# Optimization experiments

Hardware: AMD Instinct MI355X
Metric: run time of the kernel (lower is better)

Reference implementation:

```python
import jax, jax.numpy as jnp
import numpy as np

SEQ, BATCH, IN_DIM, HID, OUT = 512, 256, 300, 256, 2


def setup_inputs() -> dict:
    key = jax.random.key(0)
    ks = jax.random.split(key, 7)
    s_ih = 1.0 / np.sqrt(HID)
    return {
        "x": jax.random.normal(ks[0], (SEQ, BATCH, IN_DIM), jnp.float32),
        "W_ih": jax.random.uniform(ks[1], (HID, IN_DIM), jnp.float32, -s_ih, s_ih),
        "W_hh": jax.random.uniform(ks[2], (HID, HID), jnp.float32, -s_ih, s_ih),
        "b_ih": jax.random.uniform(ks[3], (HID,), jnp.float32, -s_ih, s_ih),
        "b_hh": jax.random.uniform(ks[4], (HID,), jnp.float32, -s_ih, s_ih),
        "W_fc": jax.random.uniform(ks[5], (OUT, HID), jnp.float32, -s_ih, s_ih),
        "b_fc": jax.random.uniform(ks[6], (OUT,), jnp.float32, -s_ih, s_ih),
    }


def reference(x, W_ih, W_hh, b_ih, b_hh, W_fc, b_fc):
    # Precompute input projection for all timesteps at once: [T, B, H]
    xp = jnp.einsum('tbi,hi->tbh', x, W_ih) + b_ih + b_hh

    def step(h, xt):
        h_new = jnp.tanh(xt + h @ W_hh.T)
        return h_new, None

    h0 = jnp.zeros((x.shape[1], W_hh.shape[0]), x.dtype)
    hT, _ = jax.lax.scan(step, h0, xp)  # hT: [B, H]
    # Dropout(0.3) is identity in eval mode.
    logits = hT @ W_fc.T + b_fc  # [B, 2]
    return jax.nn.log_softmax(logits, axis=-1)
```

## Files before the change

kernel.cpp:

```cpp
#include <hip/hip_runtime.h>
#include <hip/hip_bf16.h>
#include <cstdint>
#include <cstddef>

#define SEQ 512
#define BATCH 256
#define IN_DIM 300
#define HID 256

typedef __attribute__((ext_vector_type(8))) short bf16x8;
typedef __attribute__((ext_vector_type(4))) float f32x4;
typedef __attribute__((ext_vector_type(4))) unsigned int u32x4;

__device__ __forceinline__ unsigned short f2bf(float f) {
  union { float f; unsigned int u; } v; v.f = f;
  unsigned int u = v.u;
  return (unsigned short)((u + 0x7fffu + ((u >> 16) & 1u)) >> 16);
}
__device__ __forceinline__ unsigned short f2bf_fast(float f) {
  union { float f; unsigned int u; } v; v.f = f;
  return (unsigned short)((v.u + 0x8000u) >> 16);
}
__device__ __forceinline__ float bitsf(unsigned int u) {
  union { unsigned int u; float f; } v; v.u = u; return v.f;
}
__device__ __forceinline__ unsigned int cvtpk(float lo, float hi) {
  union { __hip_bfloat162 h; unsigned int u; } c;
  c.h = __float22bfloat162_rn(make_float2(lo, hi));
  return c.u;
}
__device__ __forceinline__ bf16x8 cvt8(float a0,float a1,float a2,float a3,
                                       float a4,float a5,float a6,float a7) {
  union { __hip_bfloat162 h2[4]; bf16x8 v; } c;
  c.h2[0] = __float22bfloat162_rn(make_float2(a0, a1));
  c.h2[1] = __float22bfloat162_rn(make_float2(a2, a3));
  c.h2[2] = __float22bfloat162_rn(make_float2(a4, a5));
  c.h2[3] = __float22bfloat162_rn(make_float2(a6, a7));
  return c.v;
}
__device__ __forceinline__ void barrier_lgkm() {
  asm volatile("s_waitcnt lgkmcnt(0)" ::: "memory");
  __builtin_amdgcn_s_barrier();
  asm volatile("" ::: "memory");
}

struct F8 { float v[8]; };
__device__ __forceinline__ F8 load_x8(const float* __restrict__ xrow, int k0, int ac) {
  F8 r;
  if (k0 + ac + 8 <= IN_DIM) {
    float2 p0 = *(const float2*)(xrow + k0 + ac + 0);
    float2 p1 = *(const float2*)(xrow + k0 + ac + 2);
    float2 p2 = *(const float2*)(xrow + k0 + ac + 4);
    float2 p3 = *(const float2*)(xrow + k0 + ac + 6);
    r.v[0]=p0.x; r.v[1]=p0.y; r.v[2]=p1.x; r.v[3]=p1.y;
    r.v[4]=p2.x; r.v[5]=p2.y; r.v[6]=p3.x; r.v[7]=p3.y;
  } else {
    #pragma unroll
    for (int j = 0; j < 8; ++j)
      r.v[j] = (k0 + ac + j < IN_DIM) ? xrow[k0 + ac + j] : 0.f;
  }
  return r;
}

__global__ __launch_bounds__(256) void conv_wih(const float* __restrict__ w,
                                                unsigned short* __restrict__ w_bf) {
  int idx = blockIdx.x * 256 + threadIdx.x;
  int j    = idx & 7;
  int l15  = (idx >> 3) & 15;
  int quad = (idx >> 7) & 3;
  int t    = idx >> 9;
  int n16  = t / 10;
  int kc   = t - n16 * 10;
  int n = n16 * 16 + l15;
  int k = kc * 32 + quad * 8 + j;
  float v = (k < IN_DIM) ? w[n * IN_DIM + k] : 0.f;
  w_bf[idx] = f2bf(v);
}

__global__ __launch_bounds__(512, 2) void gemm_xp(const float* __restrict__ x,
    const unsigned short* __restrict__ w_bf, const float* __restrict__ b_ih,
    const float* __restrict__ b_hh, unsigned int* __restrict__ xp2)
{
  __shared__ unsigned int a_lds[2][128][20];
  const int tid  = threadIdx.x;
  const int wave = tid >> 6;
  const int lane = tid & 63;
  const int l15  = lane & 15;
  const int quad = lane >> 4;
  const long m0  = (long)blockIdx.x * 128;

  bf16x8 wf[2][10];
  #pragma unroll
  for (int nt = 0; nt < 2; ++nt) {
    const unsigned short* wp =
        w_bf + ((size_t)((wave*2 + nt)*10)*4 + quad)*16*8 + (size_t)l15*8;
    #pragma unroll
    for (int kc = 0; kc < 10; ++kc)
      wf[nt][kc] = *(const bf16x8*)(wp + (size_t)kc*4*16*8);
  }

  f32x4 acc[8][2];
  #pragma unroll
  for (int mt = 0; mt < 8; ++mt) {
    acc[mt][0] = (f32x4){0.f, 0.f, 0.f, 0.f};
    acc[mt][1] = (f32x4){0.f, 0.f, 0.f, 0.f};
  }

  const int ar = tid >> 2;
  const int ac = (tid & 3) * 8;
  const float* xrow = x + (size_t)(m0 + ar) * IN_DIM;

  F8 av[2];
  av[0] = load_x8(xrow, 0, ac);
  av[1] = load_x8(xrow, 32, ac);
  {
    u32x4 pk;
    pk.x = cvtpk(av[0].v[0], av[0].v[1]);
    pk.y = cvtpk(av[0].v[2], av[0].v[3]);
    pk.z = cvtpk(av[0].v[4], av[0].v[5]);
    pk.w = cvtpk(av[0].v[6], av[0].v[7]);
    *(u32x4*)&a_lds[0][ar][(tid & 3) * 4] = pk;
  }
  barrier_lgkm();

  #pragma unroll
  for (int kc = 0; kc < 10; ++kc) {
    const int cur = kc & 1;
    bf16x8 afr[8];
    #pragma unroll
    for (int mt = 0; mt < 8; ++mt)
      afr[mt] = *(const bf16x8*)&a_lds[cur][mt*16 + l15][quad*4];
    if (kc < 9) {
      const int s = (kc + 1) & 1;
      u32x4 pk;
      pk.x = cvtpk(av[s].v[0], av[s].v[1]);
      pk.y = cvtpk(av[s].v[2], av[s].v[3]);
      pk.z = cvtpk(av[s].v[4], av[s].v[5]);
      pk.w = cvtpk(av[s].v[6], av[s].v[7]);
      *(u32x4*)&a_lds[s][ar][(tid & 3) * 4] = pk;
    }
    if (kc < 8)
      av[kc & 1] = load_x8(xrow, (kc + 2) * 32, ac);
    #pragma unroll
    for (int mt = 0; mt < 8; ++mt) {
      acc[mt][0] = __builtin_amdgcn_mfma_f32_16x16x32_bf16(afr[mt], wf[0][kc], acc[mt][0], 0, 0, 0);
      acc[mt][1] = __builtin_amdgcn_mfma_f32_16x16x32_bf16(afr[mt], wf[1][kc], acc[mt][1], 0, 0, 0);
    }
    barrier_lgkm();
  }

  const int t  = (int)(blockIdx.x >> 1);
  const int b4 = ((int)blockIdx.x & 1) * 32;
  #pragma unroll
  for (int nt = 0; nt < 2; ++nt) {
    const int n = wave*32 + nt*16 + l15;
    const float kb = 2.0f * (b_ih[n] + b_hh[n]);
    const int tid_lo = wave*64 + nt*16 + l15;
    #pragma unroll
    for (int mt = 0; mt < 8; ++mt) {
      const int g = b4 + mt*4 + quad;
      const size_t base = ((size_t)t*64 + g) * 512;
      float y0 = fmaf(2.0f, acc[mt][nt][0], kb);
      float y1 = fmaf(2.0f, acc[mt][nt][1], kb);
      float y2 = fmaf(2.0f, acc[mt][nt][2], kb);
      float y3 = fmaf(2.0f, acc[mt][nt][3], kb);
      xp2[base + tid_lo]      = cvtpk(y0, y1);
      xp2[base + tid_lo + 32] = cvtpk(y2, y3);
    }
  }
}

__global__ __launch_bounds__(512) void rnn_scan(const float* __restrict__ W_hh,
    const unsigned int* __restrict__ xp2, float* __restrict__ hT)
{
  __shared__ alignas(16) unsigned short hbuf[2][4 * 272];
  const int tid  = threadIdx.x;
  const int wave = tid >> 6;
  const int lane = tid & 63;
  const int l15  = lane & 15;
  const int quad = lane >> 4;
  const int g = blockIdx.x;
  const int c0 = wave * 32;

  bf16x8 wf[2][8];
  #pragma unroll
  for (int nt = 0; nt < 2; ++nt) {
    const int n = c0 + nt*16 + l15;
    #pragma unroll
    for (int kc = 0; kc < 8; ++kc) {
      const float* src = W_hh + n*HID + kc*32 + quad*8;
      float4 p0 = *(const float4*)src;
      float4 p1 = *(const float4*)(src + 4);
      wf[nt][kc] = cvt8(p0.x,p0.y,p0.z,p0.w,p1.x,p1.y,p1.z,p1.w);
    }
  }

  const int rb    = (quad >> 1) * 2;
  const int col_e = c0 + (quad & 1) * 16 + l15;
  const int abase = (l15 & 3) * 272 + quad * 8;

  for (int i = tid; i < 4 * 272; i += 512) hbuf[0][i] = 0;

  const unsigned int* xbase = xp2 + (size_t)g * 512 + tid;

  __syncthreads();

  unsigned int xq[16], xqn[16];
  #pragma unroll
  for (int j = 0; j < 16; ++j)
    xq[j] = xbase[(size_t)j * 32768];

  for (int tc = 0; tc < SEQ / 16; ++tc) {
    if (tc < SEQ/16 - 1) {
      const unsigned int* pn = xbase + (size_t)(tc + 1) * 16 * 32768;
      #pragma unroll
      for (int j = 0; j < 16; ++j)
        xqn[j] = pn[(size_t)j * 32768];
    }
    #pragma unroll
    for (int j = 0; j < 16; ++j) {
      const int cur = j & 1;
      bf16x8 afr[8];
      #pragma unroll
      for (int kc = 0; kc < 8; ++kc)
        afr[kc] = *(const bf16x8*)&hbuf[cur][abase + kc*32];
      f32x4 a0A = (f32x4){0.f,0.f,0.f,0.f}, a0B = a0A, a1A = a0A, a1B = a0A;
      #pragma unroll
      for (int kc = 0; kc < 8; kc += 2) {
        a0A = __builtin_amdgcn_mfma_f32_16x16x32_bf16(afr[kc],   wf[0][kc],   a0A, 0, 0, 0);
        a1A = __builtin_amdgcn_mfma_f32_16x16x32_bf16(afr[kc],   wf[1][kc],   a1A, 0, 0, 0);
        a0B = __builtin_amdgcn_mfma_f32_16x16x32_bf16(afr[kc+1], wf[0][kc+1], a0B, 0, 0, 0);
        a1B = __builtin_amdgcn_mfma_f32_16x16x32_bf16(afr[kc+1], wf[1][kc+1], a1B, 0, 0, 0);
      }
      f32x4 acc0 = a0A + a0B;
      f32x4 acc1 = a1A + a1B;
      f32x4 a = (quad & 1) ? acc1 : acc0;
      float s0 = (quad >> 1) ? a[2] : a[0];
      float s1 = (quad >> 1) ? a[3] : a[1];
      float xv0 = bitsf(xq[j] << 16);
      float xv1 = bitsf(xq[j] & 0xffff0000u);
      float y0 = fmaf(2.0f, s0, xv0);
      float y1 = fmaf(2.0f, s1, xv1);
      float h0 = fmaf(-2.0f, __builtin_amdgcn_rcpf(__expf(y0) + 1.0f), 1.0f);
      float h1 = fmaf(-2.0f, __builtin_amdgcn_rcpf(__expf(y1) + 1.0f), 1.0f);
      if (j < 15 || tc < SEQ/16 - 1) {
        hbuf[1 - cur][ rb      * 272 + col_e] = f2bf_fast(h0);
        hbuf[1 - cur][(rb + 1) * 272 + col_e] = f2bf_fast(h1);
      } else {
        hT[(size_t)(g*4 + rb    ) * HID + col_e] = h0;
        hT[(size_t)(g*4 + rb + 1) * HID + col_e] = h1;
      }
      barrier_lgkm();
    }
    if (tc < SEQ/16 - 1) {
      #pragma unroll
      for (int j = 0; j < 16; ++j)
        xq[j] = xqn[j];
    }
  }
}

__global__ __launch_bounds__(64) void fc_head(const float* __restrict__ hT,
    const float* __restrict__ W_fc, const float* __restrict__ b_fc,
    float* __restrict__ out)
{
  const int b = blockIdx.x;
  const int l = threadIdx.x;
  float s0 = 0.f, s1 = 0.f;
  #pragma unroll
  for (int j0 = 0; j0 < HID; j0 += 64) {
    float h = hT[(size_t)b * HID + j0 + l];
    s0 += h * W_fc[j0 + l];
    s1 += h * W_fc[HID + j0 + l];
  }
  #pragma unroll
  for (int off = 32; off > 0; off >>= 1) {
    s0 += __shfl_xor(s0, off, 64);
    s1 += __shfl_xor(s1, off, 64);
  }
  if (l == 0) {
    float l0 = s0 + b_fc[0], l1 = s1 + b_fc[1];
    float m = fmaxf(l0, l1);
    float lse = m + logf(expf(l0 - m) + expf(l1 - m));
    out[b*2 + 0] = l0 - lse;
    out[b*2 + 1] = l1 - lse;
  }
}

extern "C" void kernel_launch(void* const* d_in, const int* in_sizes, int n_in,
                              void* d_out, int out_size, void* d_ws, size_t ws_size,
                              hipStream_t stream) {
  const float* x    = (const float*)d_in[0];
  const float* W_ih = (const float*)d_in[1];
  const float* W_hh = (const float*)d_in[2];
  const float* b_ih = (const float*)d_in[3];
  const float* b_hh = (const float*)d_in[4];
  const float* W_fc = (const float*)d_in[5];
  const float* b_fc = (const float*)d_in[6];
  float* out = (float*)d_out;

  const size_t xp_bytes = (size_t)SEQ * BATCH * HID * 2;
  const size_t wb_bytes = (size_t)256 * 320 * 2;
  const size_t ht_bytes = (size_t)BATCH * HID * 4;
  if (ws_size < xp_bytes + wb_bytes + ht_bytes) return;

  char* ws = (char*)d_ws;
  unsigned int*   xp2  = (unsigned int*)ws;
  unsigned short* w_bf = (unsigned short*)(ws + xp_bytes);
  float*          hT   = (float*)(ws + xp_bytes + wb_bytes);

  hipLaunchKernelGGL(conv_wih, dim3(320),  dim3(256), 0, stream, W_ih, w_bf);
  hipLaunchKernelGGL(gemm_xp,  dim3(1024), dim3(512), 0, stream, x, w_bf, b_ih, b_hh, xp2);
  hipLaunchKernelGGL(rnn_scan, dim3(64),   dim3(512), 0, stream, W_hh, xp2, hT);
  hipLaunchKernelGGL(fc_head,  dim3(BATCH), dim3(64), 0, stream, hT, W_fc, b_fc, out);
}
```

Before: 482.9 us.

## Halve rnn_scan waves, giving each wave four N-tiles of the recurrent matmul

The recurrent scan block shrinks from 8 waves to 4, and each wave now holds four 16-column tiles of W_hh in registers instead of two. This doubles the MFMA work per wave per timestep. The goal is to cut the cost of the per-step block barrier and LDS traffic on the serial critical path, since fewer waves synchronize each step. The trade-off is more serial MFMA and tanh work per wave and higher register pressure, which may lengthen each step.

Measured after the change: 561.5 us. 1.16x slower.

```diff
diff --git a/kernel.cpp b/kernel.cpp
--- a/kernel.cpp
+++ b/kernel.cpp
@@ -170,7 +170,7 @@
   }
 }
 
-__global__ __launch_bounds__(512) void rnn_scan(const float* __restrict__ W_hh,
+__global__ __launch_bounds__(256, 1) void rnn_scan(const float* __restrict__ W_hh,
     const unsigned int* __restrict__ xp2, float* __restrict__ hT)
 {
   __shared__ alignas(16) unsigned short hbuf[2][4 * 272];
@@ -180,12 +180,12 @@
   const int l15  = lane & 15;
   const int quad = lane >> 4;
   const int g = blockIdx.x;
-  const int c0 = wave * 32;
-
-  bf16x8 wf[2][8];
-  #pragma unroll
-  for (int nt = 0; nt < 2; ++nt) {
-    const int n = c0 + nt*16 + l15;
+
+  bf16x8 wf[4][8];
+  #pragma unroll
+  for (int nt = 0; nt < 4; ++nt) {
+    const int n16 = 2*wave + (nt & 1) + (nt >> 1) * 8;
+    const int n = n16 * 16 + l15;
     #pragma unroll
     for (int kc = 0; kc < 8; ++kc) {
       const float* src = W_hh + n*HID + kc*32 + quad*8;
@@ -196,10 +196,10 @@
   }
 
   const int rb    = (quad >> 1) * 2;
-  const int col_e = c0 + (quad & 1) * 16 + l15;
+  const int col_e = 32*wave + (quad & 1) * 16 + l15;
   const int abase = (l15 & 3) * 272 + quad * 8;
 
-  for (int i = tid; i < 4 * 272; i += 512) hbuf[0][i] = 0;
+  for (int i = tid; i < 4 * 272; i += 256) hbuf[0][i] = 0;
 
   const unsigned int* xbase = xp2 + (size_t)g * 512 + tid;
 
@@ -207,52 +207,74 @@
 
   unsigned int xq[16], xqn[16];
   #pragma unroll
-  for (int j = 0; j < 16; ++j)
-    xq[j] = xbase[(size_t)j * 32768];
-
-  for (int tc = 0; tc < SEQ / 16; ++tc) {
-    if (tc < SEQ/16 - 1) {
-      const unsigned int* pn = xbase + (size_t)(tc + 1) * 16 * 32768;
+  for (int j = 0; j < 8; ++j) {
+    xq[2*j]   = xbase[(size_t)j * 32768];
+    xq[2*j+1] = xbase[(size_t)j * 32768 + 256];
+  }
+
+  for (int tc = 0; tc < SEQ / 8; ++tc) {
+    if (tc < SEQ/8 - 1) {
+      const unsigned int* pn = xbase + (size_t)(tc + 1) * 8 * 32768;
       #pragma unroll
-      for (int j = 0; j < 16; ++j)
-        xqn[j] = pn[(size_t)j * 32768];
-    }
-    #pragma unroll
-    for (int j = 0; j < 16; ++j) {
+      for (int j = 0; j < 8; ++j) {
+        xqn[2*j]   = pn[(size_t)j * 32768];
+        xqn[2*j+1] = pn[(size_t)j * 32768 + 256];
+      }
+    }
+    #pragma unroll
+    for (int j = 0; j < 8; ++j) {
       const int cur = j & 1;
       bf16x8 afr[8];
       #pragma unroll
       for (int kc = 0; kc < 8; ++kc)
         afr[kc] = *(const bf16x8*)&hbuf[cur][abase + kc*32];
-      f32x4 a0A = (f32x4){0.f,0.f,0.f,0.f}, a0B = a0A, a1A = a0A, a1B = a0A;
+      f32x4 z = (f32x4){0.f,0.f,0.f,0.f};
+      f32x4 aA0 = z, aA1 = z, aA2 = z, aA3 = z;
+      f32x4 aB0 = z, aB1 = z, aB2 = z, aB3 = z;
       #pragma unroll
       for (int kc = 0; kc < 8; kc += 2) {
-        a0A = __builtin_amdgcn_mfma_f32_16x16x32_bf16(afr[kc],   wf[0][kc],   a0A, 0, 0, 0);
-        a1A = __builtin_amdgcn_mfma_f32_16x16x32_bf16(afr[kc],   wf[1][kc],   a1A, 0, 0, 0);
-        a0B = __builtin_amdgcn_mfma_f32_16x16x32_bf16(afr[kc+1], wf[0][kc+1], a0B, 0, 0, 0);
-        a1B = __builtin_amdgcn_mfma_f32_16x16x32_bf16(afr[kc+1], wf[1][kc+1], a1B, 0, 0, 0);
+        aA0 = __builtin_amdgcn_mfma_f32_16x16x32_bf16(afr[kc],   wf[0][kc],   aA0, 0, 0, 0);
+        aA1 = __builtin_amdgcn_mfma_f32_16x16x32_bf16(afr[kc],   wf[1][kc],   aA1, 0, 0, 0);
+        aA2 = __builtin_amdgcn_mfma_f32_16x16x32_bf16(afr[kc],   wf[2][kc],   aA2, 0, 0, 0);
+        aA3 = __builtin_amdgcn_mfma_f32_16x16x32_bf16(afr[kc],   wf[3][kc],   aA3, 0, 0, 0);
+        aB0 = __builtin_amdgcn_mfma_f32_16x16x32_bf16(afr[kc+1], wf[0][kc+1], aB0, 0, 0, 0);
+        aB1 = __builtin_amdgcn_mfma_f32_16x16x32_bf16(afr[kc+1], wf[1][kc+1], aB1, 0, 0, 0);
+        aB2 = __builtin_amdgcn_mfma_f32_16x16x32_bf16(afr[kc+1], wf[2][kc+1], aB2, 0, 0, 0);
+        aB3 = __builtin_amdgcn_mfma_f32_16x16x32_bf16(afr[kc+1], wf[3][kc+1], aB3, 0, 0, 0);
       }
-      f32x4 acc0 = a0A + a0B;
-      f32x4 acc1 = a1A + a1B;
-      f32x4 a = (quad & 1) ? acc1 : acc0;
-      float s0 = (quad >> 1) ? a[2] : a[0];
-      float s1 = (quad >> 1) ? a[3] : a[1];
-      float xv0 = bitsf(xq[j] << 16);
-      float xv1 = bitsf(xq[j] & 0xffff0000u);
-      float y0 = fmaf(2.0f, s0, xv0);
-      float y1 = fmaf(2.0f, s1, xv1);
-      float h0 = fmaf(-2.0f, __builtin_amdgcn_rcpf(__expf(y0) + 1.0f), 1.0f);
-      float h1 = fmaf(-2.0f, __builtin_amdgcn_rcpf(__expf(y1) + 1.0f), 1.0f);
-      if (j < 15 || tc < SEQ/16 - 1) {
-        hbuf[1 - cur][ rb      * 272 + col_e] = f2bf_fast(h0);
-        hbuf[1 - cur][(rb + 1) * 272 + col_e] = f2bf_fast(h1);
+      f32x4 s0 = aA0 + aB0;
+      f32x4 s1 = aA1 + aB1;
+      f32x4 s2 = aA2 + aB2;
+      f32x4 s3 = aA3 + aB3;
+      f32x4 lo = (quad & 1) ? s1 : s0;
+      f32x4 hi = (quad & 1) ? s3 : s2;
+      float v00 = (quad >> 1) ? lo[2] : lo[0];
+      float v10 = (quad >> 1) ? lo[3] : lo[1];
+      float v01 = (quad >> 1) ? hi[2] : hi[0];
+      float v11 = (quad >> 1) ? hi[3] : hi[1];
+      const unsigned int xlo = xq[2*j], xhi = xq[2*j+1];
+      float y00 = fmaf(2.0f, v00, bitsf(xlo << 16));
+      float y10 = fmaf(2.0f, v10, bitsf(xlo & 0xffff0000u));
+      float y01 = fmaf(2.0f, v01, bitsf(xhi << 16));
+      float y11 = fmaf(2.0f, v11, bitsf(xhi & 0xffff0000u));
+      float h00 = fmaf(-2.0f, __builtin_amdgcn_rcpf(__expf(y00) + 1.0f), 1.0f);
+      float h10 = fmaf(-2.0f, __builtin_amdgcn_rcpf(__expf(y10) + 1.0f), 1.0f);
+      float h01 = fmaf(-2.0f, __builtin_amdgcn_rcpf(__expf(y01) + 1.0f), 1.0f);
+      float h11 = fmaf(-2.0f, __builtin_amdgcn_rcpf(__expf(y11) + 1.0f), 1.0f);
+      if (j < 7 || tc < SEQ/8 - 1) {
+        hbuf[1 - cur][ rb      * 272 + col_e      ] = f2bf_fast(h00);
+        hbuf[1 - cur][(rb + 1) * 272 + col_e      ] = f2bf_fast(h10);
+        hbuf[1 - cur][ rb      * 272 + col_e + 128] = f2bf_fast(h01);
+        hbuf[1 - cur][(rb + 1) * 272 + col_e + 128] = f2bf_fast(h11);
       } else {
-        hT[(size_t)(g*4 + rb    ) * HID + col_e] = h0;
-        hT[(size_t)(g*4 + rb + 1) * HID + col_e] = h1;
+        hT[(size_t)(g*4 + rb    ) * HID + col_e      ] = h00;
+        hT[(size_t)(g*4 + rb + 1) * HID + col_e      ] = h10;
+        hT[(size_t)(g*4 + rb    ) * HID + col_e + 128] = h01;
+        hT[(size_t)(g*4 + rb + 1) * HID + col_e + 128] = h11;
       }
       barrier_lgkm();
     }
-    if (tc < SEQ/16 - 1) {
+    if (tc < SEQ/8 - 1) {
       #pragma unroll
       for (int j = 0; j < 16; ++j)
         xq[j] = xqn[j];
@@ -311,6 +333,6 @@
 
   hipLaunchKernelGGL(conv_wih, dim3(320),  dim3(256), 0, stream, W_ih, w_bf);
   hipLaunchKernelGGL(gemm_xp,  dim3(1024), dim3(512), 0, stream, x, w_bf, b_ih, b_hh, xp2);
-  hipLaunchKernelGGL(rnn_scan, dim3(64),   dim3(512), 0, stream, W_hh, xp2, hT);
+  hipLaunchKernelGGL(rnn_scan, dim3(64),   dim3(256), 0, stream, W_hh, xp2, hT);
   hipLaunchKernelGGL(fc_head,  dim3(BATCH), dim3(64), 0, stream, hT, W_fc, b_fc, out);
 }
```

## Fuse input-projection GEMM and RNN scan with per-timestep completion flags

Applied to the files above, without the earlier changes.

Merges the xp GEMM and the recurrent scan into one launch. The first 64 blocks run the scan and the remaining 1024 blocks compute the input projection, each signalling a per-timestep done counter via an atomic add. Scan blocks spin-wait on the counters for each 16-step window before loading xp, so the serial scan can start while the GEMM is still producing later timesteps. The risk is spin-wait overhead and a dependence on the 64 scan blocks being resident alongside the GEMM blocks; if block scheduling does not guarantee that, the kernel could deadlock.

Measured after the change: 552.7 us. +14.5%, slower.

```diff
diff --git a/kernel.cpp b/kernel.cpp
--- a/kernel.cpp
+++ b/kernel.cpp
@@ -40,6 +40,11 @@
 }
 __device__ __forceinline__ void barrier_lgkm() {
   asm volatile("s_waitcnt lgkmcnt(0)" ::: "memory");
+  __builtin_amdgcn_s_barrier();
+  asm volatile("" ::: "memory");
+}
+__device__ __forceinline__ void barrier_raw() {
+  asm volatile("" ::: "memory");
   __builtin_amdgcn_s_barrier();
   asm volatile("" ::: "memory");
 }
@@ -63,8 +68,10 @@
 }
 
 __global__ __launch_bounds__(256) void conv_wih(const float* __restrict__ w,
-                                                unsigned short* __restrict__ w_bf) {
+                                                unsigned short* __restrict__ w_bf,
+                                                unsigned int* __restrict__ done) {
   int idx = blockIdx.x * 256 + threadIdx.x;
+  if (idx < SEQ) done[idx] = 0;
   int j    = idx & 7;
   int l15  = (idx >> 3) & 15;
   int quad = (idx >> 7) & 3;
@@ -77,108 +84,129 @@
   w_bf[idx] = f2bf(v);
 }
 
-__global__ __launch_bounds__(512, 2) void gemm_xp(const float* __restrict__ x,
+__device__ __forceinline__ void wait_window(const unsigned int* __restrict__ done, int w) {
+  if (w < SEQ / 16) {
+    if (threadIdx.x == 0) {
+      const int t0 = w * 16;
+      #pragma unroll 1
+      for (int i = 0; i < 16; ++i)
+        while (__hip_atomic_load(&done[t0 + i], __ATOMIC_RELAXED,
+                                 __HIP_MEMORY_SCOPE_AGENT) < 2u)
+          __builtin_amdgcn_s_sleep(8);
+      __threadfence();
+    }
+    barrier_raw();
+  }
+}
+
+__global__ __launch_bounds__(512, 2) void rnn_fused(const float* __restrict__ x,
     const unsigned short* __restrict__ w_bf, const float* __restrict__ b_ih,
-    const float* __restrict__ b_hh, unsigned int* __restrict__ xp2)
+    const float* __restrict__ b_hh, const float* __restrict__ W_hh,
+    unsigned int* __restrict__ xp2, float* __restrict__ hT,
+    unsigned int* __restrict__ done)
 {
-  __shared__ unsigned int a_lds[2][128][20];
+  __shared__ alignas(16) unsigned char lds_raw[20480];
   const int tid  = threadIdx.x;
   const int wave = tid >> 6;
   const int lane = tid & 63;
   const int l15  = lane & 15;
   const int quad = lane >> 4;
-  const long m0  = (long)blockIdx.x * 128;
-
-  bf16x8 wf[2][10];
-  #pragma unroll
-  for (int nt = 0; nt < 2; ++nt) {
-    const unsigned short* wp =
-        w_bf + ((size_t)((wave*2 + nt)*10)*4 + quad)*16*8 + (size_t)l15*8;
-    #pragma unroll
-    for (int kc = 0; kc < 10; ++kc)
-      wf[nt][kc] = *(const bf16x8*)(wp + (size_t)kc*4*16*8);
-  }
-
-  f32x4 acc[8][2];
-  #pragma unroll
-  for (int mt = 0; mt < 8; ++mt) {
-    acc[mt][0] = (f32x4){0.f, 0.f, 0.f, 0.f};
-    acc[mt][1] = (f32x4){0.f, 0.f, 0.f, 0.f};
-  }
-
-  const int ar = tid >> 2;
-  const int ac = (tid & 3) * 8;
-  const float* xrow = x + (size_t)(m0 + ar) * IN_DIM;
-
-  F8 av[2];
-  av[0] = load_x8(xrow, 0, ac);
-  av[1] = load_x8(xrow, 32, ac);
-  {
-    u32x4 pk;
-    pk.x = cvtpk(av[0].v[0], av[0].v[1]);
-    pk.y = cvtpk(av[0].v[2], av[0].v[3]);
-    pk.z = cvtpk(av[0].v[4], av[0].v[5]);
-    pk.w = cvtpk(av[0].v[6], av[0].v[7]);
-    *(u32x4*)&a_lds[0][ar][(tid & 3) * 4] = pk;
-  }
-  barrier_lgkm();
-
-  #pragma unroll
-  for (int kc = 0; kc < 10; ++kc) {
-    const int cur = kc & 1;
-    bf16x8 afr[8];
-    #pragma unroll
-    for (int mt = 0; mt < 8; ++mt)
-      afr[mt] = *(const bf16x8*)&a_lds[cur][mt*16 + l15][quad*4];
-    if (kc < 9) {
-      const int s = (kc + 1) & 1;
+
+  if (blockIdx.x >= 64) {
+    typedef unsigned int ALds[128][20];
+    ALds* a_lds = (ALds*)lds_raw;
+    const int bx = (int)blockIdx.x - 64;
+    const long m0 = (long)bx * 128;
+
+    bf16x8 wf[2][10];
+    #pragma unroll
+    for (int nt = 0; nt < 2; ++nt) {
+      const unsigned short* wp =
+          w_bf + ((size_t)((wave*2 + nt)*10)*4 + quad)*16*8 + (size_t)l15*8;
+      #pragma unroll
+      for (int kc = 0; kc < 10; ++kc)
+        wf[nt][kc] = *(const bf16x8*)(wp + (size_t)kc*4*16*8);
+    }
+
+    f32x4 acc[8][2];
+    #pragma unroll
+    for (int mt = 0; mt < 8; ++mt) {
+      acc[mt][0] = (f32x4){0.f, 0.f, 0.f, 0.f};
+      acc[mt][1] = (f32x4){0.f, 0.f, 0.f, 0.f};
+    }
+
+    const int ar = tid >> 2;
+    const int ac = (tid & 3) * 8;
+    const float* xrow = x + (size_t)(m0 + ar) * IN_DIM;
+
+    F8 av[2];
+    av[0] = load_x8(xrow, 0, ac);
+    av[1] = load_x8(xrow, 32, ac);
+    {
       u32x4 pk;
-      pk.x = cvtpk(av[s].v[0], av[s].v[1]);
-      pk.y = cvtpk(av[s].v[2], av[s].v[3]);
-      pk.z = cvtpk(av[s].v[4], av[s].v[5]);
-      pk.w = cvtpk(av[s].v[6], av[s].v[7]);
-      *(u32x4*)&a_lds[s][ar][(tid & 3) * 4] = pk;
-    }
-    if (kc < 8)
-      av[kc & 1] = load_x8(xrow, (kc + 2) * 32, ac);
-    #pragma unroll
-    for (int mt = 0; mt < 8; ++mt) {
-      acc[mt][0] = __builtin_amdgcn_mfma_f32_16x16x32_bf16(afr[mt], wf[0][kc], acc[mt][0], 0, 0, 0);
-      acc[mt][1] = __builtin_amdgcn_mfma_f32_16x16x32_bf16(afr[mt], wf[1][kc], acc[mt][1], 0, 0, 0);
+      pk.x = cvtpk(av[0].v[0], av[0].v[1]);
+      pk.y = cvtpk(av[0].v[2], av[0].v[3]);
+      pk.z = cvtpk(av[0].v[4], av[0].v[5]);
+      pk.w = cvtpk(av[0].v[6], av[0].v[7]);
+      *(u32x4*)&a_lds[0][ar][(tid & 3) * 4] = pk;
     }
     barrier_lgkm();
-  }
-
-  const int t  = (int)(blockIdx.x >> 1);
-  const int b4 = ((int)blockIdx.x & 1) * 32;
-  #pragma unroll
-  for (int nt = 0; nt < 2; ++nt) {
-    const int n = wave*32 + nt*16 + l15;
-    const float kb = 2.0f * (b_ih[n] + b_hh[n]);
-    const int tid_lo = wave*64 + nt*16 + l15;
-    #pragma unroll
-    for (int mt = 0; mt < 8; ++mt) {
-      const int g = b4 + mt*4 + quad;
-      const size_t base = ((size_t)t*64 + g) * 512;
-      float y0 = fmaf(2.0f, acc[mt][nt][0], kb);
-      float y1 = fmaf(2.0f, acc[mt][nt][1], kb);
-      float y2 = fmaf(2.0f, acc[mt][nt][2], kb);
-      float y3 = fmaf(2.0f, acc[mt][nt][3], kb);
-      xp2[base + tid_lo]      = cvtpk(y0, y1);
-      xp2[base + tid_lo + 32] = cvtpk(y2, y3);
-    }
-  }
-}
-
-__global__ __launch_bounds__(512) void rnn_scan(const float* __restrict__ W_hh,
-    const unsigned int* __restrict__ xp2, float* __restrict__ hT)
-{
-  __shared__ alignas(16) unsigned short hbuf[2][4 * 272];
-  const int tid  = threadIdx.x;
-  const int wave = tid >> 6;
-  const int lane = tid & 63;
-  const int l15  = lane & 15;
-  const int quad = lane >> 4;
+
+    #pragma unroll
+    for (int kc = 0; kc < 10; ++kc) {
+      const int cur = kc & 1;
+      bf16x8 afr[8];
+      #pragma unroll
+      for (int mt = 0; mt < 8; ++mt)
+        afr[mt] = *(const bf16x8*)&a_lds[cur][mt*16 + l15][quad*4];
+      if (kc < 9) {
+        const int s = (kc + 1) & 1;
+        u32x4 pk;
+        pk.x = cvtpk(av[s].v[0], av[s].v[1]);
+        pk.y = cvtpk(av[s].v[2], av[s].v[3]);
+        pk.z = cvtpk(av[s].v[4], av[s].v[5]);
+        pk.w = cvtpk(av[s].v[6], av[s].v[7]);
+        *(u32x4*)&a_lds[s][ar][(tid & 3) * 4] = pk;
+      }
+      if (kc < 8)
+        av[kc & 1] = load_x8(xrow, (kc + 2) * 32, ac);
+      #pragma unroll
+      for (int mt = 0; mt < 8; ++mt) {
+        acc[mt][0] = __builtin_amdgcn_mfma_f32_16x16x32_bf16(afr[mt], wf[0][kc], acc[mt][0], 0, 0, 0);
+        acc[mt][1] = __builtin_amdgcn_mfma_f32_16x16x32_bf16(afr[mt], wf[1][kc], acc[mt][1], 0, 0, 0);
+      }
+      barrier_lgkm();
+    }
+
+    const int t  = bx >> 1;
+    const int b4 = (bx & 1) * 32;
+    #pragma unroll
+    for (int nt = 0; nt < 2; ++nt) {
+      const int n = wave*32 + nt*16 + l15;
+      const float kb = 2.0f * (b_ih[n] + b_hh[n]);
+      const int tid_lo = wave*64 + nt*16 + l15;
+      #pragma unroll
+      for (int mt = 0; mt < 8; ++mt) {
+        const int g = b4 + mt*4 + quad;
+        const size_t base = ((size_t)t*64 + g) * 512;
+        float y0 = fmaf(2.0f, acc[mt][nt][0], kb);
+        float y1 = fmaf(2.0f, acc[mt][nt][1], kb);
+        float y2 = fmaf(2.0f, acc[mt][nt][2], kb);
+        float y3 = fmaf(2.0f, acc[mt][nt][3], kb);
+        xp2[base + tid_lo]      = cvtpk(y0, y1);
+        xp2[base + tid_lo + 32] = cvtpk(y2, y3);
+      }
+    }
+    __syncthreads();
+    if (tid == 0) {
+      __threadfence();
+      __hip_atomic_fetch_add(&done[t], 1u, __ATOMIC_RELAXED, __HIP_MEMORY_SCOPE_AGENT);
+    }
+    return;
+  }
+
+  typedef unsigned short HBuf[4 * 272];
+  HBuf* hbuf = (HBuf*)lds_raw;
   const int g = blockIdx.x;
   const int c0 = wave * 32;
 
@@ -206,11 +234,14 @@
   __syncthreads();
 
   unsigned int xq[16], xqn[16];
+  wait_window(done, 0);
   #pragma unroll
   for (int j = 0; j < 16; ++j)
     xq[j] = xbase[(size_t)j * 32768];
+  wait_window(done, 1);
 
   for (int tc = 0; tc < SEQ / 16; ++tc) {
+    wait_window(done, tc + 2);
     if (tc < SEQ/16 - 1) {
       const unsigned int* pn = xbase + (size_t)(tc + 1) * 16 * 32768;
       #pragma unroll
@@ -302,15 +333,17 @@
   const size_t xp_bytes = (size_t)SEQ * BATCH * HID * 2;
   const size_t wb_bytes = (size_t)256 * 320 * 2;
   const size_t ht_bytes = (size_t)BATCH * HID * 4;
-  if (ws_size < xp_bytes + wb_bytes + ht_bytes) return;
+  const size_t dn_bytes = (size_t)SEQ * 4;
+  if (ws_size < xp_bytes + wb_bytes + ht_bytes + dn_bytes) return;
 
   char* ws = (char*)d_ws;
   unsigned int*   xp2  = (unsigned int*)ws;
   unsigned short* w_bf = (unsigned short*)(ws + xp_bytes);
   float*          hT   = (float*)(ws + xp_bytes + wb_bytes);
-
-  hipLaunchKernelGGL(conv_wih, dim3(320),  dim3(256), 0, stream, W_ih, w_bf);
-  hipLaunchKernelGGL(gemm_xp,  dim3(1024), dim3(512), 0, stream, x, w_bf, b_ih, b_hh, xp2);
-  hipLaunchKernelGGL(rnn_scan, dim3(64),   dim3(512), 0, stream, W_hh, xp2, hT);
-  hipLaunchKernelGGL(fc_head,  dim3(BATCH), dim3(64), 0, stream, hT, W_fc, b_fc, out);
-}
+  unsigned int*   done = (unsigned int*)(ws + xp_bytes + wb_bytes + ht_bytes);
+
+  hipLaunchKernelGGL(conv_wih,  dim3(320),   dim3(256), 0, stream, W_ih, w_bf, done);
+  hipLaunchKernelGGL(rnn_fused, dim3(1088),  dim3(512), 0, stream,
+                     x, w_bf, b_ih, b_hh, W_hh, xp2, hT, done);
+  hipLaunchKernelGGL(fc_head,   dim3(BATCH), dim3(64),  0, stream, hT, W_fc, b_fc, out);
+}
```
